# Performance work log

Hardware: AMD Instinct MI355X
Metric: run time of the kernel (lower is better)

The kernel has to match this reference:

```python
import jax, jax.numpy as jnp
import numpy as np
from jax import lax

B, T, C, H, W = 2, 5, 2, 128, 256
E, M, L = 64, 16, 4  # embedding_dim, n_fno_modes, n_fno_layers
EPS = 1e-5


def conv1x1(x, w, b):
    # x: [N, I, H, W], w: [O, I], b: [O]
    return jnp.einsum('nihw,oi->nohw', x, w) + b[None, :, None, None]


def conv3x3(x, w, b):
    # x: [N, I, H, W], w: [O, I, 3, 3]
    y = lax.conv_general_dilated(x, w, window_strides=(1, 1), padding='SAME',
                                 dimension_numbers=('NCHW', 'OIHW', 'NCHW'))
    return y + b[None, :, None, None]


def instance_norm(x):
    # InstanceNorm2d(affine=False): normalize over H,W per (n, c), biased var
    mu = jnp.mean(x, axis=(2, 3), keepdims=True)
    var = jnp.var(x, axis=(2, 3), keepdims=True)
    return (x - mu) * lax.rsqrt(var + EPS)


def upsample2x_nearest(x):
    return jnp.repeat(jnp.repeat(x, 2, axis=2), 2, axis=3)


def resize_nearest(x, out_h, out_w):
    # torch F.interpolate mode='nearest': idx = floor(i * in / out)
    in_h, in_w = x.shape[2], x.shape[3]
    hi = (jnp.arange(out_h) * in_h) // out_h
    wi = (jnp.arange(out_w) * in_w) // out_w
    return x[:, :, hi, :][:, :, :, wi]


def fno_layer(x, wr, wi, cw, cb):
    # x: [N, E, H, W]; wr/wi: [2, E, E, M, M]; cw: [E, E]; cb: [E]
    h, w = x.shape[2], x.shape[3]
    coeff = jnp.fft.rfft2(x, axes=(2, 3), norm='ortho')  # [N, E, H, W//2+1]
    w0 = wr[0] + 1j * wi[0]
    w1 = wr[1] + 1j * wi[1]
    out = jnp.zeros_like(coeff)
    out = out.at[:, :, :M, :M].set(
        jnp.einsum('nixy,ioxy->noxy', coeff[:, :, :M, :M], w0))
    out = out.at[:, :, -M:, :M].set(
        jnp.einsum('nixy,ioxy->noxy', coeff[:, :, -M:, :M], w1))
    spec = jnp.fft.irfft2(out, s=(h, w), axes=(2, 3), norm='ortho')
    return jax.nn.gelu(conv1x1(x, cw, cb) + spec, approximate=False)


def setup_inputs() -> dict:
    key = jax.random.key(0)
    ks = jax.random.split(key, 10)
    s = 0.02
    return {
        'sensor_value': jax.random.normal(ks[0], (B, T, C, H, W), jnp.float32),
        'updim_w': 0.3 * jax.random.normal(ks[1], (E, C), jnp.float32),
        'updim_b': jnp.zeros((E,), jnp.float32),
        'smooth_w': 0.04 * jax.random.normal(ks[2], (E, E, 3, 3), jnp.float32),
        'smooth_b': jnp.zeros((E,), jnp.float32),
        'fno_wr': s * jax.random.normal(ks[3], (L, 2, E, E, M, M), jnp.float32),
        'fno_wi': s * jax.random.normal(ks[4], (L, 2, E, E, M, M), jnp.float32),
        'fno_cw': 0.1 * jax.random.normal(ks[5], (L, E, E), jnp.float32),
        'fno_cb': jnp.zeros((L, E), jnp.float32),
        'downdim_w': 0.1 * jax.random.normal(ks[6], (C, E), jnp.float32),
        'downdim_b': jnp.zeros((C,), jnp.float32),
    }


def reference(sensor_value, updim_w, updim_b, smooth_w, smooth_b,
              fno_wr, fno_wi, fno_cw, fno_cb, downdim_w, downdim_b):
    b, t, c, h, w = sensor_value.shape
    x = sensor_value.reshape(b * t, c, h, w)
    x = conv1x1(x, updim_w, updim_b)
    x = upsample2x_nearest(x)
    x = jax.nn.gelu(instance_norm(conv3x3(x, smooth_w, smooth_b)), approximate=False)
    x = resize_nearest(x, H, W)
    for l in range(L):
        x = fno_layer(x, fno_wr[l], fno_wi[l], fno_cw[l], fno_cb[l])
    x = conv1x1(x, downdim_w, downdim_b)
    return x.reshape(b, t, c, H, W)
```

## Files before the change

### kernel.cpp

```cpp
#include <hip/hip_runtime.h>
#include <math.h>

#define PI_D 3.14159265358979323846


typedef _Float16 h8 __attribute__((ext_vector_type(8)));
typedef float f16v __attribute__((ext_vector_type(16)));

__device__ __forceinline__ float gelu_f(float v){
  return 0.5f*v*(1.0f + erff(v*0.70710678118654752440f));
}

__device__ __forceinline__ int fsw_c(int w){ return (w ^ (w >> 3)) & 7; }

__global__ __launch_bounds__(256) void k_tables_fold(float* __restrict__ twFwH, float* __restrict__ twBwH,
                                                     _Float16* __restrict__ Tspec, _Float16* __restrict__ TdftW,
                                                     const float* __restrict__ smw, const float* __restrict__ upw,
                                                     const float* __restrict__ upb, float* __restrict__ Keff){
  int bid = blockIdx.x;
  if (bid < 96){
    int id = bid*256 + threadIdx.x;
    if (id < 4096){
      int h = id >> 5, m = id & 31;
      int xm = (m < 16) ? m : (96 + m);
      double ang = -2.0*PI_D*(double)((xm*h) & 127)/128.0;
      twFwH[id*2]   = (float)cos(ang);
      twFwH[id*2+1] = (float)sin(ang);
    } else if (id < 8192){
      int j = id - 4096;
      int h = j >> 5, m = j & 31;
      int xm = (m < 16) ? m : (96 + m);
      double ang = 2.0*PI_D*(double)((xm*h) & 127)/128.0;
      twBwH[j*2]   = (float)cos(ang);
      twBwH[j*2+1] = (float)sin(ang);
    } else if (id < 16384){
      int j = id - 8192;
      int w = j >> 5, kk = j & 31;
      int y = kk >> 1;
      double ang = 2.0*PI_D*(double)((w*y) & 255)/256.0;
      double v = (kk & 1) ? -sin(ang) : cos(ang);
      Tspec[j] = (_Float16)v;
    } else if (id < 24576){
      int j = id - 16384;
      int y2 = j >> 8, w = j & 255;
      int y = y2 >> 1;
      double ang = -2.0*PI_D*(double)((w*y) & 255)/256.0;
      double v = (y2 & 1) ? sin(ang) : cos(ang);
      TdftW[j] = (_Float16)v;
    }
  } else {
    int id = (bid-96)*256 + threadIdx.x;
    if (id >= 1024) return;
    int o = id >> 4, rs = (id >> 2) & 3, tap = id & 3;
    int r = rs >> 1, s = rs & 1, a = tap >> 1, b = tap & 1;
    int klo = (r==0) ? (a==0?0:1) : (a==0?0:2);
    int khi = (r==0) ? (a==0?0:2) : (a==0?1:2);
    int llo = (s==0) ? (b==0?0:1) : (b==0?0:2);
    int lhi = (s==0) ? (b==0?0:2) : (b==0?1:2);
    float a0=0.f, a1=0.f, ab=0.f;
    for (int i=0;i<64;++i){
      float t = 0.f;
      for (int kh=klo; kh<=khi; ++kh)
        for (int kw=llo; kw<=lhi; ++kw)
          t += smw[((size_t)o*64+i)*9 + kh*3+kw];
      a0 += t*upw[i*2];
      a1 += t*upw[i*2+1];
      ab += t*upb[i];
    }
    *(float4*)(Keff + o*64 + (rs*4+tap)*4) = make_float4(a0, a1, ab, 0.f);
  }
}

__global__ __launch_bounds__(256) void k_transW(const float* __restrict__ wr, const float* __restrict__ wi,
                                                unsigned* __restrict__ Wt){
  __shared__ unsigned P[64*257];
  int lb = blockIdx.x;
  int i = lb & 63, blk = (lb>>6)&1, l = lb>>7;
  int tid = threadIdx.x;
  size_t sbase = (size_t)l*2097152 + (size_t)blk*1048576 + (size_t)i*16384 + tid;
  for (int o=0;o<64;++o){
    float a = wr[sbase + (size_t)o*256];
    float b = wi[sbase + (size_t)o*256];
    union { unsigned u; _Float16 h[2]; } pk;
    pk.h[0] = (_Float16)a; pk.h[1] = (_Float16)b;
    P[o*257 + tid] = pk.u;
  }
  __syncthreads();
  int o = tid & 63, g = tid >> 6;
  size_t dbase = (size_t)(l*2+blk)*1048576;
  for (int it=0; it<64; ++it){
    int my = g*64 + it;
    Wt[dbase + (size_t)my*4096 + i*64 + o] = P[o*257 + my];
  }
}

__global__ __launch_bounds__(512) void k_corrbnd(const float* __restrict__ sv, float* __restrict__ Rpart,
                                                 float* __restrict__ Bnd){
  __shared__ float SH[3120];
  int bid = blockIdx.x;
  int tid = threadIdx.x;
  if (bid < 320){
    int band = bid & 31, n = bid >> 5;
    int u0 = band*4;
    for (int t = tid; t < 3120; t += 512){
      int ch = t / 1560; int rem = t - ch*1560; int rr = rem / 260; int ci = rem - rr*260;
      int row = u0 - 1 + rr, col = ci - 1;
      float v = 0.f;
      if (row >= 0 && row < 128 && col >= 0 && col < 256)
        v = sv[((size_t)(n*2+ch)*128 + row)*256 + col];
      SH[(ch*6+rr)*260 + ci] = v;
    }
    __syncthreads();

    int lane = tid & 63, wv = tid >> 6;
    int c  = (wv<4) ? (wv>>1) : ((wv<6) ? (wv-4) : 2);
    int c2 = (wv<4) ? (wv&1)  : ((wv<6) ? 2 : (wv-6));
    float acc[9];
    #pragma unroll
    for (int k=0;k<9;++k) acc[k]=0.f;

    for (int r=0;r<4;++r){
      int u = u0 + r, lu = r + 1;
      for (int cb=0;cb<4;++cb){
        int v = cb*64 + lane;
        float f = (c==2) ? 1.f : SH[(c*6+lu)*260 + 1+v];
        #pragma unroll
        for (int dr=-1;dr<=1;++dr){
          int ur = u + dr;
          float rko = (ur>=0 && ur<128) ? 1.f : 0.f;
          #pragma unroll
          for (int dc=-1;dc<=1;++dc){
            float g;
            if (c2==2){
              int vc = v + dc;
              g = rko * ((vc>=0 && vc<256) ? 1.f : 0.f);
            } else {
              g = SH[(c2*6+lu+dr)*260 + 1+v+dc];
            }
            acc[(dr+1)*3 + dc+1] += f*g;
          }
        }
      }
    }
    #pragma unroll
    for (int k=0;k<9;++k){
      float v = acc[k];
      for (int off=32; off; off>>=1) v += __shfl_xor(v, off);
      if (lane==0) Rpart[((size_t)(n*32+band)*8 + wv)*9 + k] = v;
    }
  } else {
    int n = bid - 320;
    for (int t = tid; t < 3120; t += 512){
      int e = t/780; int rem = t - e*780; int ch = rem/260; int i = rem - ch*260;
      int idx = i - 1;
      int len = (e<2) ? 256 : 128;
      float v = 0.f;
      if (idx >= 0 && idx < len){
        if (ch==2) v = 1.f;
        else {
          int row = (e==0) ? 0 : (e==1) ? 127 : idx;
          int col = (e==2) ? 0 : (e==3) ? 255 : idx;
          v = sv[((size_t)(n*2+ch)*128 + row)*256 + col];
        }
      }
      SH[(e*3+ch)*260 + i] = v;
    }
    __syncthreads();
    if (tid < 108){
      int e = tid/27; int rem = tid - e*27; int pair = rem/3; int lag = rem%3 - 1;
      int c = pair/3, c2 = pair%3;
      int len = (e<2) ? 256 : 128;
      float a = 0.f;
      for (int i=0;i<len;++i) a += SH[(e*3+c)*260 + 1+i]*SH[(e*3+c2)*260 + 1+i+lag];
      Bnd[n*144 + tid] = a;
    } else if (tid < 144){
      int t = tid - 108; int corner = t/9; int pair = t - corner*9;
      int c = pair/3, c2 = pair%3;
      int e = (corner<2) ? 0 : 1;
      int idx = (corner&1) ? 255 : 0;
      Bnd[n*144 + tid] = SH[(e*3+c)*260 + 1+idx]*SH[(e*3+c2)*260 + 1+idx];
    }
  }
}

__global__ __launch_bounds__(256) void k_stats3(const float* __restrict__ Rpart, const float* __restrict__ Bnd,
                                                const float* __restrict__ Keff, float* __restrict__ stats){
  __shared__ float R[9][9];
  __shared__ float BL[4][9][3];
  __shared__ float CR[4][9];
  __shared__ float M[4][12][12];
  int n = blockIdx.x, tid = threadIdx.x;

  if (tid < 72){
    int wv = tid/9, k = tid - (tid/9)*9;
    double s = 0.0;
    for (int b=0;b<32;++b) s += (double)Rpart[((size_t)(n*32+b)*8 + wv)*9 + k];
    int c  = (wv<4) ? (wv>>1) : ((wv<6) ? (wv-4) : 2);
    int c2 = (wv<4) ? (wv&1)  : ((wv<6) ? 2 : (wv-6));
    R[c*3+c2][k] = (float)s;
  } else if (tid < 81){
    int k = tid - 72; int dr = k/3 - 1, dc = k%3 - 1;
    R[8][k] = (float)((128 - (dr<0?-dr:dr)) * (256 - (dc<0?-dc:dc)));
  }
  if (tid < 108){
    int e = tid/27, rem = tid - (tid/27)*27;
    BL[e][rem/3][rem%3] = Bnd[n*144 + tid];
  } else if (tid < 144){
    int t = tid - 108;
    CR[t/9][t - (t/9)*9] = Bnd[n*144 + tid];
  }
  __syncthreads();

  for (int t = tid; t < 576; t += 256){
    int rs = t/144; int rem = t - rs*144; int i = rem/12, j = rem - (rem/12)*12;
    int ab = i/3,  c  = i - ab*3,  a  = ab>>1, b  = ab&1;
    int ab2 = j/3, c2 = j - ab2*3, a2 = ab2>>1, b2 = ab2&1;
    int r = rs>>1, s = rs&1;
    int dr = a2 - a, dc = b2 - b;
    int pair = c*3 + c2;
    float g = R[pair][(dr+1)*3 + (dc+1)];
    if (r==1 && a==1 && a2==1) g -= BL[0][pair][dc+1];
    if (r==0 && a==0 && a2==0) g -= BL[1][pair][dc+1];
    if (s==1 && b==1 && b2==1) g -= BL[2][pair][dr+1];
    if (s==0 && b==0 && b2==0) g -= BL[3][pair][dr+1];
    bool rowc = (a==a2) && ((r==1 && a==1) || (r==0 && a==0));
    bool colc = (b==b2) && ((s==1 && b==1) || (s==0 && b==0));
    if (rowc && colc){
      int corner = ((r==1)?0:2) + ((s==1)?0:1);
      g += CR[corner][pair];
    }
    M[rs][i][j] = g;
  }
  __syncthreads();

  if (tid < 64){
    int o = tid;
    double S1 = 0.0, S2 = 0.0;
    for (int rs=0; rs<4; ++rs){
      float w[12];
      #pragma unroll
      for (int ab=0; ab<4; ++ab){
        float4 kv = *(const float4*)(Keff + o*64 + (rs*4+ab)*4);
        w[ab*3+0] = kv.x; w[ab*3+1] = kv.y; w[ab*3+2] = kv.z;
      }
      #pragma unroll
      for (int i=0;i<12;++i){
        double ti = 0.0;
        #pragma unroll
        for (int j=0;j<12;++j) ti += (double)M[rs][i][j]*(double)w[j];
        S2 += (double)w[i]*ti;
      }
      #pragma unroll
      for (int ab=0; ab<4; ++ab)
        #pragma unroll
        for (int c=0;c<3;++c)
          S1 += (double)w[ab*3+c]*(double)M[rs][ab*3+c][ab*3+2];
    }
    double mu  = S1 / 131072.0;
    double var = S2 / 131072.0 - mu*mu;
    stats[(n*64+o)*2]   = (float)mu;
    stats[(n*64+o)*2+1] = (float)(1.0/sqrt(var + 1e-5));
  }
}

__global__ __launch_bounds__(256) void k_convnorm(const float* __restrict__ sv,
                                                  const float* __restrict__ Keff,
                                                  const float* __restrict__ stats,
                                                  _Float16* __restrict__ act){
  __shared__ float SV[4*260];
  int bid = blockIdx.x;
  int p = bid & 127, n = bid >> 7;
  int tid = threadIdx.x;
  for (int t = tid; t < 1032; t += 256){
    int dr = t / 516;
    int rem = t - dr*516;
    int ch = rem / 258;
    int ci = rem - ch*258;
    int row = p - 1 + dr;
    int col = ci - 1;
    float v = 0.f;
    if (row >= 0 && col >= 0 && col < 256)
      v = sv[((size_t)(n*2+ch)*128 + row)*256 + col];
    SV[(dr*2+ch)*260 + ci] = v;
  }
  __syncthreads();

  int q = tid;
  float x0[4], x1[4], ib[4];
  float rowok0 = (p>0)?1.f:0.f;
  float colok0 = (q>0)?1.f:0.f;
  #pragma unroll
  for (int a=0;a<2;++a)
    #pragma unroll
    for (int b=0;b<2;++b){
      x0[a*2+b] = SV[(a*2+0)*260 + q + b];
      x1[a*2+b] = SV[(a*2+1)*260 + q + b];
      ib[a*2+b] = (a==0?rowok0:1.f) * (b==0?colok0:1.f);
    }

  for (int o=0; o<64; ++o){
    const float4* kp = (const float4*)(Keff + o*64);
    float y = 0.f;
    #pragma unroll
    for (int t=0;t<4;++t){
      float4 kv = kp[t];
      y += kv.x*x0[t] + kv.y*x1[t] + kv.z*ib[t];
    }
    float mu = stats[(n*64+o)*2], istd = stats[(n*64+o)*2+1];
    float v = (y - mu)*istd;
    act[((size_t)(n*64+o)*128 + p)*256 + q] = (_Float16)gelu_f(v);
  }
}

__global__ __launch_bounds__(256, 2) void k_dftW_mfma(const _Float16* __restrict__ act,
                                                      const _Float16* __restrict__ TdftW,
                                                      float* __restrict__ Cy){
  __shared__ _Float16 Ax[32768];
  __shared__ _Float16 Bt[8192];
  int tid = threadIdx.x;
  int hp = blockIdx.x & 63, n = blockIdx.x >> 6;
  int h0 = hp*2;

  {
    int a = tid >> 1;
    int ws = (tid & 1) * 128;
    int e = a & 63, ht = a >> 6;
    const _Float16* src = act + ((size_t)(n*64+e))*32768 + (size_t)(h0+ht)*256 + ws;
    #pragma unroll
    for (int k=0;k<16;++k){
      h8 v = *(const h8*)(src + k*8);
      int wq = (ws >> 3) + k;
      int chunk = wq ^ (a & 7);
      *(h8*)(Ax + a*256 + chunk*8) = v;
    }
  }
  {
    int y2 = tid & 31, ws = (tid >> 5) * 32;
    const _Float16* src = TdftW + y2*256 + ws;
    #pragma unroll
    for (int k=0;k<4;++k){
      h8 v = *(const h8*)(src + k*8);
      int wq = (ws >> 3) + k;
      int chunk = wq ^ (y2 & 7);
      *(h8*)(Bt + y2*256 + chunk*8) = v;
    }
  }
  __syncthreads();

  int lane = tid & 63;
  int l31 = lane & 31, l5 = lane >> 5;
  int mt = tid >> 6;
  int a = mt*32 + l31;

  f16v acc;
  #pragma unroll
  for (int j=0;j<16;++j) acc[j] = 0.f;
  #pragma unroll
  for (int ks=0;ks<16;++ks){
    int kb = ks*16 + l5*8;
    int cA = (kb>>3) ^ (a & 7);
    int cB = (kb>>3) ^ (l31 & 7);
    h8 af = *(const h8*)(Ax + a*256 + cA*8);
    h8 bf = *(const h8*)(Bt + l31*256 + cB*8);
    acc = __builtin_amdgcn_mfma_f32_32x32x16_f16(bf, af, acc, 0,0,0);
  }
  int e = a & 63, ht = a >> 6;
  #pragma unroll
  for (int j=0;j<16;j+=2){
    int y2 = (j&3) + 8*(j>>2) + 4*l5;
    int yy = y2 >> 1;
    *(float2*)(Cy + (((size_t)(n*16+yy)*128 + h0+ht)*64 + e)*2) = make_float2(acc[j], acc[j+1]);
  }
}

__global__ __launch_bounds__(256) void k_specAB(const float* __restrict__ Cy,
                                                const float* __restrict__ twF,
                                                const unsigned* __restrict__ Wt,
                                                float* __restrict__ MS, int l){
  __shared__ float CO[8*64*2];
  int bid = blockIdx.x;
  int mq = bid / 160;
  int pid = bid - mq*160;
  int y = pid & 15, n = pid >> 4;
  int tid = threadIdx.x;
  int lane = tid & 63;
  int wv = __builtin_amdgcn_readfirstlane(tid >> 6);

  {
    int m0 = mq*8 + wv*2;
    const float* cyb = Cy + (((size_t)(n*16+y)*128)*64 + lane)*2;
    const float* tf = twF + m0*2;
    float ar0=0.f, ai0=0.f, ar1=0.f, ai1=0.f;
    for (int h=0; h<128; ++h){
      float2 c = *(const float2*)(cyb + h*128);
      const float* tp = tf + h*64;
      float t0r = tp[0], t0i = tp[1], t1r = tp[2], t1i = tp[3];
      ar0 += t0r*c.x - t0i*c.y; ai0 += t0r*c.y + t0i*c.x;
      ar1 += t1r*c.x - t1i*c.y; ai1 += t1r*c.y + t1i*c.x;
    }
    int mm = wv*2;
    *(float2*)(CO + (mm*64 + lane)*2)     = make_float2(ar0, ai0);
    *(float2*)(CO + ((mm+1)*64 + lane)*2) = make_float2(ar1, ai1);
  }
  __syncthreads();

  {
    #pragma unroll
    for (int t2=0; t2<2; ++t2){
      int mm = wv*2 + t2;
      int m = mq*8 + mm;
      int blk = m >> 4, mloc = m & 15;
      int my = mloc*16 + y;
      const unsigned* wb = Wt + ((size_t)((l*2+blk)*256 + my))*4096 + lane;
      float mr = 0.f, mi = 0.f;
      for (int i=0;i<64;++i){
        float2 cc = *(const float2*)(CO + (mm*64 + i)*2);
        union { unsigned u; _Float16 h[2]; } pk;
        pk.u = wb[(size_t)i*64];
        float wr_f = (float)pk.h[0], wi_f = (float)pk.h[1];
        mr += cc.x*wr_f - cc.y*wi_f;
        mi += cc.x*wi_f + cc.y*wr_f;
      }
      *(float2*)(MS + (((size_t)(n*16+y)*32 + m)*64 + lane)*2) = make_float2(mr, mi);
    }
  }
}

__global__ __launch_bounds__(256) void k_specC(const float* __restrict__ MS,
                                               const float* __restrict__ twB,
                                               float* __restrict__ G){
  __shared__ float SM[32*64*2];
  int bid = blockIdx.x;
  int hq = bid / 160;
  int pid = bid - hq*160;
  int y = pid & 15, n = pid >> 4;
  int tid = threadIdx.x;
  int lane = tid & 63;
  int wv = __builtin_amdgcn_readfirstlane(tid >> 6);

  {
    const float4* src = (const float4*)(MS + ((size_t)(n*16+y)*32)*128);
    float4* dst = (float4*)SM;
    #pragma unroll
    for (int t=0; t<4; ++t) dst[tid + t*256] = src[tid + t*256];
  }
  __syncthreads();

  float f = (y==0) ? (1.f/32768.f) : (2.f/32768.f);
  for (int k=0;k<8;++k){
    int h = hq*32 + wv*8 + k;
    const float* tb = twB + h*64;
    float gr=0.f, gi=0.f;
    #pragma unroll
    for (int m=0;m<32;++m){
      float tr = tb[m*2], ti = tb[m*2+1];
      float2 mo2 = *(const float2*)(SM + (m*64+lane)*2);
      gr += tr*mo2.x - ti*mo2.y;
      gi += tr*mo2.y + ti*mo2.x;
    }
    size_t gb = (((size_t)(n*128+h)*16 + y)*2)*64 + lane;
    G[gb]      = gr*f;
    G[gb + 64] = gi*f;
  }
}

__global__ __launch_bounds__(1024, 8) void k_combine_mfma(const _Float16* __restrict__ act_in,
                                                          const float* __restrict__ G,
                                                          const _Float16* __restrict__ Tspec,
                                                          const _Float16* __restrict__ TdftW,
                                                          const float* __restrict__ cw,
                                                          const float* __restrict__ cb,
                                                          const float* __restrict__ wd,
                                                          const float* __restrict__ bd,
                                                          _Float16* __restrict__ act_out,
                                                          float* __restrict__ Cy,
                                                          float* __restrict__ outp,
                                                          int flags){
  __shared__ __align__(16) _Float16 Lh[40960];
  _Float16* Bx = Lh;
  _Float16* At = Lh + 32768;
  int tid = threadIdx.x;
  int h = blockIdx.x & 127, n = blockIdx.x >> 7;

  {
    int rp = tid >> 5, sub = tid & 31;
    int i0 = 2*rp;
    int wbase = sub*8;
    const _Float16* r0 = act_in + (size_t)(n*64+i0)*32768 + (size_t)h*256 + wbase;
    const _Float16* r1 = r0 + 32768;
    h8 A0 = *(const h8*)r0;
    h8 B0 = *(const h8*)r1;
    int cbs = rp >> 2;
    int lo  = i0 & 7;
    #pragma unroll
    for (int k=0;k<8;++k){
      union { _Float16 hh[2]; unsigned u; } pk;
      pk.hh[0] = A0[k];
      pk.hh[1] = B0[k];
      int w = wbase + k;
      int chunk = cbs ^ fsw_c(w);
      *(unsigned*)(Bx + w*128 + chunk*8 + lo) = pk.u;
    }
  }
  if (tid < 512){
    int o = tid >> 3, seg = (tid & 7)*8;
    float4 c0 = *(const float4*)(cw + o*64 + seg);
    float4 c1 = *(const float4*)(cw + o*64 + seg + 4);
    h8 v;
    v[0]=(_Float16)c0.x; v[1]=(_Float16)c0.y; v[2]=(_Float16)c0.z; v[3]=(_Float16)c0.w;
    v[4]=(_Float16)c1.x; v[5]=(_Float16)c1.y; v[6]=(_Float16)c1.z; v[7]=(_Float16)c1.w;
    int ch0 = (seg>>3) ^ (o & 7);
    *(h8*)(At + o*128 + ch0*8) = v;
  } else {
    int t5 = tid - 512;
    const float* gp = G + (size_t)(n*128 + h)*2048 + t5*4;
    float4 g = *(const float4*)gp;
    float gvx[4] = {g.x, g.y, g.z, g.w};
    int idx0 = t5*4;
    int yc = idx0 >> 6;
    int o0 = idx0 & 63;
    int kk = 64 + yc;
    #pragma unroll
    for (int j=0;j<4;++j){
      int o = o0 + j;
      int chunk = (kk >> 3) ^ (o & 7);
      At[o*128 + chunk*8 + (kk & 7)] = (_Float16)gvx[j];
    }
  }
  if (tid < 512){
    int w = tid >> 1, half = tid & 1;
    const _Float16* tp = Tspec + w*32 + half*16;
    #pragma unroll
    for (int c=0;c<2;++c){
      h8 v = *(const h8*)(tp + c*8);
      int cc = half*2 + c;
      int chunk = (8 + cc) ^ fsw_c(w);
      *(h8*)(Bx + w*128 + chunk*8) = v;
    }
  }
  __syncthreads();

  int lane = tid & 63;
  int l31 = lane & 31, l5 = lane >> 5;
  int w0i = tid >> 6;
  int mt = w0i & 1, ng = w0i >> 1;
  int o_lane = mt*32 + l31;

  h8 af[6];
  #pragma unroll
  for (int ks=0;ks<6;++ks){
    int kb = ks*16 + l5*8;
    int chunk = (kb>>3) ^ (o_lane & 7);
    af[ks] = *(const h8*)(At + o_lane*128 + chunk*8);
  }

  f16v acc;
  #pragma unroll
  for (int j=0;j<16;++j) acc[j] = cb[mt*32 + (j&3) + 8*(j>>2) + 4*l5];

  {
    int w = ng*32 + l31;
    const _Float16* bbase = Bx + w*128;
    int wf = fsw_c(w);
    #pragma unroll
    for (int ks=0;ks<6;++ks){
      int kb = ks*16 + l5*8;
      int chunk = (kb>>3) ^ wf;
      h8 bf = *(const h8*)(bbase + chunk*8);
      acc = __builtin_amdgcn_mfma_f32_32x32x16_f16(af[ks], bf, acc, 0,0,0);
    }
  }

  float gvv[16];
  #pragma unroll
  for (int j=0;j<16;++j) gvv[j] = gelu_f(acc[j]);

  int wcol = ng*32 + l31;
  if (flags != 2){
    #pragma unroll
    for (int j=0;j<16;++j){
      int o = mt*32 + (j&3) + 8*(j>>2) + 4*l5;
      act_out[(size_t)(n*64+o)*32768 + (size_t)h*256 + wcol] = (_Float16)gvv[j];
    }
  }
  __syncthreads();

  if (flags == 1){
    _Float16* gL  = Lh;
    _Float16* TdL = Lh + 16384;
    {
      int wc3 = wcol >> 3, wc7 = wcol & 7;
      #pragma unroll
      for (int j=0;j<16;++j){
        int o = mt*32 + (j&3) + 8*(j>>2) + 4*l5;
        gL[o*256 + ((wc3 ^ (o & 7))*8) + wc7] = (_Float16)gvv[j];
      }
    }
    {
      int y2 = tid & 31, ws = (tid >> 5)*8;
      const _Float16* src = TdftW + y2*256 + ws;
      h8 v = *(const h8*)src;
      int chunk = (ws>>3) ^ (y2 & 7);
      *(h8*)(TdL + y2*256 + chunk*8) = v;
    }
    __syncthreads();
    float* P = (float*)(Lh + 24576);
    if (w0i < 8){
      int mt2 = w0i & 1, kq = w0i >> 1;
      int ocol = mt2*32 + l31;
      f16v acc2;
      #pragma unroll
      for (int j=0;j<16;++j) acc2[j] = 0.f;
      #pragma unroll
      for (int ks=0;ks<4;++ks){
        int kb = (kq*4+ks)*16 + l5*8;
        h8 af2 = *(const h8*)(gL  + ocol*256 + (((kb>>3) ^ (ocol & 7))*8));
        h8 bf2 = *(const h8*)(TdL + l31*256  + (((kb>>3) ^ (l31 & 7))*8));
        acc2 = __builtin_amdgcn_mfma_f32_32x32x16_f16(bf2, af2, acc2, 0,0,0);
      }
      #pragma unroll
      for (int j=0;j<16;++j){
        int y2 = (j&3) + 8*(j>>2) + 4*l5;
        P[w0i*1024 + y2*32 + l31] = acc2[j];
      }
    }
    __syncthreads();
    {
      int yy = tid >> 6, o = tid & 63, mt2 = o >> 5, o31 = o & 31;
      float re = P[(0*2+mt2)*1024 + (2*yy)*32 + o31]   + P[(1*2+mt2)*1024 + (2*yy)*32 + o31]
               + P[(2*2+mt2)*1024 + (2*yy)*32 + o31]   + P[(3*2+mt2)*1024 + (2*yy)*32 + o31];
      float im = P[(0*2+mt2)*1024 + (2*yy+1)*32 + o31] + P[(1*2+mt2)*1024 + (2*yy+1)*32 + o31]
               + P[(2*2+mt2)*1024 + (2*yy+1)*32 + o31] + P[(3*2+mt2)*1024 + (2*yy+1)*32 + o31];
      *(float2*)(Cy + (((size_t)(n*16+yy)*128 + h)*64 + o)*2) = make_float2(re, im);
    }
  } else {
    float p0=0.f, p1=0.f;
    #pragma unroll
    for (int j=0;j<16;++j){
      int o = mt*32 + (j&3) + 8*(j>>2) + 4*l5;
      p0 += wd[o]*gvv[j];
      p1 += wd[64+o]*gvv[j];
    }
    p0 += __shfl_xor(p0,32);
    p1 += __shfl_xor(p1,32);
    float* red = (float*)(Lh + 32768);
    if (l5 == 0){
      red[wcol*4 + mt*2 + 0] = p0;
      red[wcol*4 + mt*2 + 1] = p1;
    }
    __syncthreads();
    if (tid < 512){
      int ch = tid >> 8, wc = tid & 255;
      float v = red[wc*4 + ch] + red[wc*4 + 2 + ch] + bd[ch];
      outp[(size_t)n*65536 + (size_t)ch*32768 + (size_t)h*256 + wc] = v;
    }
  }
}

extern "C" void kernel_launch(void* const* d_in, const int* in_sizes, int n_in,
                              void* d_out, int out_size, void* d_ws, size_t ws_size,
                              hipStream_t stream) {
  const float* sv  = (const float*)d_in[0];
  const float* upw = (const float*)d_in[1];
  const float* upb = (const float*)d_in[2];
  const float* smw = (const float*)d_in[3];
  const float* smb = (const float*)d_in[4];
  const float* fwr = (const float*)d_in[5];
  const float* fwi = (const float*)d_in[6];
  const float* fcw = (const float*)d_in[7];
  const float* fcb = (const float*)d_in[8];
  const float* ddw = (const float*)d_in[9];
  const float* ddb = (const float*)d_in[10];
  float* out = (float*)d_out;
  (void)smb;

  float* W = (float*)d_ws;
  _Float16* actA = (_Float16*)W;
  _Float16* actB = (_Float16*)(W + 10485760);
  float* Cy    = W + 20971520;
  float* G     = W + 23592960;
  float* part  = W + 26214400;
  float* stats = W + 28180480;
  float* Keff  = W + 28181760;
  float* twFwH = W + 28185856;
  float* twBwH = W + 28194048;
  _Float16* Tspec = (_Float16*)(W + 28202240);
  _Float16* TdftW = (_Float16*)(W + 28206336);
  unsigned* Wt   = (unsigned*)(W + 28210432);

  float* Rpart = part;
  float* Bnd   = part + 30000;
  float* MS    = part + 65536;

  k_tables_fold<<<100,256,0,stream>>>(twFwH, twBwH, Tspec, TdftW, smw, upw, upb, Keff);
  k_transW<<<512,256,0,stream>>>(fwr, fwi, Wt);
  k_corrbnd<<<330,512,0,stream>>>(sv, Rpart, Bnd);
  k_stats3<<<10,256,0,stream>>>(Rpart, Bnd, Keff, stats);
  k_convnorm<<<1280,256,0,stream>>>(sv, Keff, stats, actA);
  k_dftW_mfma<<<640,256,0,stream>>>(actA, TdftW, Cy);

  _Float16* xa = actA; _Float16* xb = actB;
  for (int l=0;l<4;++l){
    k_specAB<<<640,256,0,stream>>>(Cy, twFwH, Wt, MS, l);
    k_specC<<<640,256,0,stream>>>(MS, twBwH, G);
    k_combine_mfma<<<1280,1024,0,stream>>>(xa, G, Tspec, TdftW,
                                           fcw + (size_t)l*4096, fcb + (size_t)l*64,
                                           ddw, ddb, xb, Cy, out, (l<3)?1:2);
    _Float16* t = xa; xa = xb; xb = t;
  }
}
```

Measured before the change: 466.7 us.

## Fuse W-direction DFT into convnorm and inverse H-DFT into combine, switch to NHWC

```diff
diff --git a/kernel.cpp b/kernel.cpp
--- a/kernel.cpp
+++ b/kernel.cpp
@@ -5,6 +5,7 @@
 
 
 typedef _Float16 h8 __attribute__((ext_vector_type(8)));
+typedef _Float16 h4v __attribute__((ext_vector_type(4)));
 typedef float f16v __attribute__((ext_vector_type(16)));
 
 __device__ __forceinline__ float gelu_f(float v){
@@ -263,15 +264,21 @@
   }
 }
 
-__global__ __launch_bounds__(256) void k_convnorm(const float* __restrict__ sv,
-                                                  const float* __restrict__ Keff,
-                                                  const float* __restrict__ stats,
-                                                  _Float16* __restrict__ act){
-  __shared__ float SV[4*260];
+__global__ __launch_bounds__(1024, 8) void k_convnorm(const float* __restrict__ sv,
+                                                      const float* __restrict__ Keff,
+                                                      const float* __restrict__ stats,
+                                                      const _Float16* __restrict__ TdftW,
+                                                      _Float16* __restrict__ act,
+                                                      float* __restrict__ Cy){
+  __shared__ __align__(16) _Float16 Lh[40960];
+  _Float16* gL  = Lh;
+  _Float16* TdL = Lh + 16384;
+  float*    P   = (float*)(Lh + 24576);
+  float*    SV  = P;
   int bid = blockIdx.x;
   int p = bid & 127, n = bid >> 7;
   int tid = threadIdx.x;
-  for (int t = tid; t < 1032; t += 256){
+  for (int t = tid; t < 1032; t += 1024){
     int dr = t / 516;
     int rem = t - dr*516;
     int ch = rem / 258;
@@ -283,9 +290,17 @@
       v = sv[((size_t)(n*2+ch)*128 + row)*256 + col];
     SV[(dr*2+ch)*260 + ci] = v;
   }
-  __syncthreads();
-
-  int q = tid;
+  {
+    int y2 = tid & 31, ws = (tid >> 5)*8;
+    const _Float16* src = TdftW + y2*256 + ws;
+    h8 v = *(const h8*)src;
+    int chunk = (ws>>3) ^ (y2 & 7);
+    *(h8*)(TdL + y2*256 + chunk*8) = v;
+  }
+  __syncthreads();
+
+  int q = tid & 255;
+  int og = __builtin_amdgcn_readfirstlane(tid >> 8);
   float x0[4], x1[4], ib[4];
   float rowok0 = (p>0)?1.f:0.f;
   float colok0 = (q>0)?1.f:0.f;
@@ -298,7 +313,11 @@
       ib[a*2+b] = (a==0?rowok0:1.f) * (b==0?colok0:1.f);
     }
 
-  for (int o=0; o<64; ++o){
+  union { _Float16 g16[16]; h8 gv8[2]; } U;
+  int q3 = q>>3, q7 = q&7;
+  #pragma unroll
+  for (int oi=0; oi<16; ++oi){
+    int o = og*16 + oi;
     const float4* kp = (const float4*)(Keff + o*64);
     float y = 0.f;
     #pragma unroll
@@ -307,69 +326,47 @@
       y += kv.x*x0[t] + kv.y*x1[t] + kv.z*ib[t];
     }
     float mu = stats[(n*64+o)*2], istd = stats[(n*64+o)*2+1];
-    float v = (y - mu)*istd;
-    act[((size_t)(n*64+o)*128 + p)*256 + q] = (_Float16)gelu_f(v);
-  }
-}
-
-__global__ __launch_bounds__(256, 2) void k_dftW_mfma(const _Float16* __restrict__ act,
-                                                      const _Float16* __restrict__ TdftW,
-                                                      float* __restrict__ Cy){
-  __shared__ _Float16 Ax[32768];
-  __shared__ _Float16 Bt[8192];
-  int tid = threadIdx.x;
-  int hp = blockIdx.x & 63, n = blockIdx.x >> 6;
-  int h0 = hp*2;
-
-  {
-    int a = tid >> 1;
-    int ws = (tid & 1) * 128;
-    int e = a & 63, ht = a >> 6;
-    const _Float16* src = act + ((size_t)(n*64+e))*32768 + (size_t)(h0+ht)*256 + ws;
-    #pragma unroll
-    for (int k=0;k<16;++k){
-      h8 v = *(const h8*)(src + k*8);
-      int wq = (ws >> 3) + k;
-      int chunk = wq ^ (a & 7);
-      *(h8*)(Ax + a*256 + chunk*8) = v;
-    }
-  }
-  {
-    int y2 = tid & 31, ws = (tid >> 5) * 32;
-    const _Float16* src = TdftW + y2*256 + ws;
-    #pragma unroll
-    for (int k=0;k<4;++k){
-      h8 v = *(const h8*)(src + k*8);
-      int wq = (ws >> 3) + k;
-      int chunk = wq ^ (y2 & 7);
-      *(h8*)(Bt + y2*256 + chunk*8) = v;
-    }
+    _Float16 gh = (_Float16)gelu_f((y - mu)*istd);
+    U.g16[oi] = gh;
+    gL[o*256 + ((q3 ^ (o & 7))*8) + q7] = gh;
+  }
+  {
+    _Float16* ap = act + (((size_t)(n*128+p)*256 + q)*64 + og*16);
+    *(h8*)ap = U.gv8[0];
+    *(h8*)(ap+8) = U.gv8[1];
   }
   __syncthreads();
 
   int lane = tid & 63;
   int l31 = lane & 31, l5 = lane >> 5;
-  int mt = tid >> 6;
-  int a = mt*32 + l31;
-
-  f16v acc;
-  #pragma unroll
-  for (int j=0;j<16;++j) acc[j] = 0.f;
-  #pragma unroll
-  for (int ks=0;ks<16;++ks){
-    int kb = ks*16 + l5*8;
-    int cA = (kb>>3) ^ (a & 7);
-    int cB = (kb>>3) ^ (l31 & 7);
-    h8 af = *(const h8*)(Ax + a*256 + cA*8);
-    h8 bf = *(const h8*)(Bt + l31*256 + cB*8);
-    acc = __builtin_amdgcn_mfma_f32_32x32x16_f16(bf, af, acc, 0,0,0);
-  }
-  int e = a & 63, ht = a >> 6;
-  #pragma unroll
-  for (int j=0;j<16;j+=2){
-    int y2 = (j&3) + 8*(j>>2) + 4*l5;
-    int yy = y2 >> 1;
-    *(float2*)(Cy + (((size_t)(n*16+yy)*128 + h0+ht)*64 + e)*2) = make_float2(acc[j], acc[j+1]);
+  int w0i = tid >> 6;
+  if (w0i < 8){
+    int mt2 = w0i & 1, kq = w0i >> 1;
+    int ocol = mt2*32 + l31;
+    f16v acc2;
+    #pragma unroll
+    for (int j=0;j<16;++j) acc2[j] = 0.f;
+    #pragma unroll
+    for (int ks=0;ks<4;++ks){
+      int kb = (kq*4+ks)*16 + l5*8;
+      h8 af2 = *(const h8*)(gL  + ocol*256 + (((kb>>3) ^ (ocol & 7))*8));
+      h8 bf2 = *(const h8*)(TdL + l31*256  + (((kb>>3) ^ (l31 & 7))*8));
+      acc2 = __builtin_amdgcn_mfma_f32_32x32x16_f16(bf2, af2, acc2, 0,0,0);
+    }
+    #pragma unroll
+    for (int j=0;j<16;++j){
+      int y2 = (j&3) + 8*(j>>2) + 4*l5;
+      P[w0i*1024 + y2*32 + l31] = acc2[j];
+    }
+  }
+  __syncthreads();
+  {
+    int yy = tid >> 6, o = tid & 63, mt2 = o >> 5, o31 = o & 31;
+    float re = P[(0*2+mt2)*1024 + (2*yy)*32 + o31]   + P[(1*2+mt2)*1024 + (2*yy)*32 + o31]
+             + P[(2*2+mt2)*1024 + (2*yy)*32 + o31]   + P[(3*2+mt2)*1024 + (2*yy)*32 + o31];
+    float im = P[(0*2+mt2)*1024 + (2*yy+1)*32 + o31] + P[(1*2+mt2)*1024 + (2*yy+1)*32 + o31]
+             + P[(2*2+mt2)*1024 + (2*yy+1)*32 + o31] + P[(3*2+mt2)*1024 + (2*yy+1)*32 + o31];
+    *(float2*)(Cy + (((size_t)(n*16+yy)*128 + p)*64 + o)*2) = make_float2(re, im);
   }
 }
 
@@ -405,6 +402,7 @@
   __syncthreads();
 
   {
+    float f = (y==0) ? (1.f/32768.f) : (2.f/32768.f);
     #pragma unroll
     for (int t2=0; t2<2; ++t2){
       int mm = wv*2 + t2;
@@ -421,53 +419,16 @@
         mr += cc.x*wr_f - cc.y*wi_f;
         mi += cc.x*wi_f + cc.y*wr_f;
       }
-      *(float2*)(MS + (((size_t)(n*16+y)*32 + m)*64 + lane)*2) = make_float2(mr, mi);
-    }
-  }
-}
-
-__global__ __launch_bounds__(256) void k_specC(const float* __restrict__ MS,
-                                               const float* __restrict__ twB,
-                                               float* __restrict__ G){
-  __shared__ float SM[32*64*2];
-  int bid = blockIdx.x;
-  int hq = bid / 160;
-  int pid = bid - hq*160;
-  int y = pid & 15, n = pid >> 4;
-  int tid = threadIdx.x;
-  int lane = tid & 63;
-  int wv = __builtin_amdgcn_readfirstlane(tid >> 6);
-
-  {
-    const float4* src = (const float4*)(MS + ((size_t)(n*16+y)*32)*128);
-    float4* dst = (float4*)SM;
-    #pragma unroll
-    for (int t=0; t<4; ++t) dst[tid + t*256] = src[tid + t*256];
-  }
-  __syncthreads();
-
-  float f = (y==0) ? (1.f/32768.f) : (2.f/32768.f);
-  for (int k=0;k<8;++k){
-    int h = hq*32 + wv*8 + k;
-    const float* tb = twB + h*64;
-    float gr=0.f, gi=0.f;
-    #pragma unroll
-    for (int m=0;m<32;++m){
-      float tr = tb[m*2], ti = tb[m*2+1];
-      float2 mo2 = *(const float2*)(SM + (m*64+lane)*2);
-      gr += tr*mo2.x - ti*mo2.y;
-      gi += tr*mo2.y + ti*mo2.x;
-    }
-    size_t gb = (((size_t)(n*128+h)*16 + y)*2)*64 + lane;
-    G[gb]      = gr*f;
-    G[gb + 64] = gi*f;
+      *(float2*)(MS + (((size_t)(n*16+y)*32 + m)*64 + lane)*2) = make_float2(mr*f, mi*f);
+    }
   }
 }
 
 __global__ __launch_bounds__(1024, 8) void k_combine_mfma(const _Float16* __restrict__ act_in,
-                                                          const float* __restrict__ G,
+                                                          const float* __restrict__ MS,
                                                           const _Float16* __restrict__ Tspec,
                                                           const _Float16* __restrict__ TdftW,
+                                                          const float* __restrict__ twB,
                                                           const float* __restrict__ cw,
                                                           const float* __restrict__ cb,
                                                           const float* __restrict__ wd,
@@ -482,25 +443,30 @@
   int tid = threadIdx.x;
   int h = blockIdx.x & 127, n = blockIdx.x >> 7;
 
-  {
-    int rp = tid >> 5, sub = tid & 31;
-    int i0 = 2*rp;
-    int wbase = sub*8;
-    const _Float16* r0 = act_in + (size_t)(n*64+i0)*32768 + (size_t)h*256 + wbase;
-    const _Float16* r1 = r0 + 32768;
-    h8 A0 = *(const h8*)r0;
-    h8 B0 = *(const h8*)r1;
-    int cbs = rp >> 2;
-    int lo  = i0 & 7;
-    #pragma unroll
-    for (int k=0;k<8;++k){
-      union { _Float16 hh[2]; unsigned u; } pk;
-      pk.hh[0] = A0[k];
-      pk.hh[1] = B0[k];
-      int w = wbase + k;
-      int chunk = cbs ^ fsw_c(w);
-      *(unsigned*)(Bx + w*128 + chunk*8 + lo) = pk.u;
-    }
+  int wA = tid >> 2, ksg = tid & 3;
+  const _Float16* asrc = act_in + (((size_t)(n*128+h)*256 + wA)*64 + ksg*16);
+  h8 av0 = *(const h8*)asrc;
+  h8 av1 = *(const h8*)(asrc + 8);
+
+  int o_g = tid & 63;
+  int yv = __builtin_amdgcn_readfirstlane(tid >> 6);
+  float gr = 0.f, gi = 0.f;
+  {
+    const float* ms = MS + (size_t)(n*16+yv)*4096 + o_g*2;
+    const float* tb = twB + h*64;
+    #pragma unroll 4
+    for (int m=0;m<32;++m){
+      float tr = tb[m*2], ti = tb[m*2+1];
+      float2 mo = *(const float2*)(ms + m*128);
+      gr += tr*mo.x - ti*mo.y;
+      gi += tr*mo.y + ti*mo.x;
+    }
+  }
+
+  {
+    int fw = fsw_c(wA);
+    *(h8*)(Bx + wA*128 + ((ksg*2)   ^ fw)*8) = av0;
+    *(h8*)(Bx + wA*128 + ((ksg*2+1) ^ fw)*8) = av1;
   }
   if (tid < 512){
     int o = tid >> 3, seg = (tid & 7)*8;
@@ -513,30 +479,21 @@
     *(h8*)(At + o*128 + ch0*8) = v;
   } else {
     int t5 = tid - 512;
-    const float* gp = G + (size_t)(n*128 + h)*2048 + t5*4;
-    float4 g = *(const float4*)gp;
-    float gvx[4] = {g.x, g.y, g.z, g.w};
-    int idx0 = t5*4;
-    int yc = idx0 >> 6;
-    int o0 = idx0 & 63;
-    int kk = 64 + yc;
-    #pragma unroll
-    for (int j=0;j<4;++j){
-      int o = o0 + j;
-      int chunk = (kk >> 3) ^ (o & 7);
-      At[o*128 + chunk*8 + (kk & 7)] = (_Float16)gvx[j];
-    }
-  }
-  if (tid < 512){
-    int w = tid >> 1, half = tid & 1;
+    int w = t5 >> 1, half = t5 & 1;
     const _Float16* tp = Tspec + w*32 + half*16;
+    int fw = fsw_c(w);
     #pragma unroll
     for (int c=0;c<2;++c){
       h8 v = *(const h8*)(tp + c*8);
       int cc = half*2 + c;
-      int chunk = (8 + cc) ^ fsw_c(w);
-      *(h8*)(Bx + w*128 + chunk*8) = v;
-    }
+      *(h8*)(Bx + w*128 + ((8 + cc) ^ fw)*8) = v;
+    }
+  }
+  {
+    int kk0 = 64 + 2*yv;
+    At[o_g*128 + (((kk0>>3) ^ (o_g & 7))*8) + (kk0 & 7)] = (_Float16)gr;
+    int kk1 = kk0 + 1;
+    At[o_g*128 + (((kk1>>3) ^ (o_g & 7))*8) + (kk1 & 7)] = (_Float16)gi;
   }
   __syncthreads();
 
@@ -558,10 +515,10 @@
   #pragma unroll
   for (int j=0;j<16;++j) acc[j] = cb[mt*32 + (j&3) + 8*(j>>2) + 4*l5];
 
-  {
-    int w = ng*32 + l31;
-    const _Float16* bbase = Bx + w*128;
-    int wf = fsw_c(w);
+  int wcol = ng*32 + l31;
+  {
+    const _Float16* bbase = Bx + wcol*128;
+    int wf = fsw_c(wcol);
     #pragma unroll
     for (int ks=0;ks<6;++ks){
       int kb = ks*16 + l5*8;
@@ -575,12 +532,14 @@
   #pragma unroll
   for (int j=0;j<16;++j) gvv[j] = gelu_f(acc[j]);
 
-  int wcol = ng*32 + l31;
   if (flags != 2){
-    #pragma unroll
-    for (int j=0;j<16;++j){
-      int o = mt*32 + (j&3) + 8*(j>>2) + 4*l5;
-      act_out[(size_t)(n*64+o)*32768 + (size_t)h*256 + wcol] = (_Float16)gvv[j];
+    _Float16* ab = act_out + (((size_t)(n*128+h)*256 + wcol)*64 + mt*32 + 4*l5);
+    #pragma unroll
+    for (int g=0;g<4;++g){
+      h4v v4;
+      v4[0]=(_Float16)gvv[g*4+0]; v4[1]=(_Float16)gvv[g*4+1];
+      v4[2]=(_Float16)gvv[g*4+2]; v4[3]=(_Float16)gvv[g*4+3];
+      *(h4v*)(ab + 8*g) = v4;
     }
   }
   __syncthreads();
@@ -678,7 +637,6 @@
   _Float16* actA = (_Float16*)W;
   _Float16* actB = (_Float16*)(W + 10485760);
   float* Cy    = W + 20971520;
-  float* G     = W + 23592960;
   float* part  = W + 26214400;
   float* stats = W + 28180480;
   float* Keff  = W + 28181760;
@@ -696,14 +654,12 @@
   k_transW<<<512,256,0,stream>>>(fwr, fwi, Wt);
   k_corrbnd<<<330,512,0,stream>>>(sv, Rpart, Bnd);
   k_stats3<<<10,256,0,stream>>>(Rpart, Bnd, Keff, stats);
-  k_convnorm<<<1280,256,0,stream>>>(sv, Keff, stats, actA);
-  k_dftW_mfma<<<640,256,0,stream>>>(actA, TdftW, Cy);
+  k_convnorm<<<1280,1024,0,stream>>>(sv, Keff, stats, TdftW, actA, Cy);
 
   _Float16* xa = actA; _Float16* xb = actB;
   for (int l=0;l<4;++l){
     k_specAB<<<640,256,0,stream>>>(Cy, twFwH, Wt, MS, l);
-    k_specC<<<640,256,0,stream>>>(MS, twBwH, G);
-    k_combine_mfma<<<1280,1024,0,stream>>>(xa, G, Tspec, TdftW,
+    k_combine_mfma<<<1280,1024,0,stream>>>(xa, MS, Tspec, TdftW, twBwH,
                                            fcw + (size_t)l*4096, fcb + (size_t)l*64,
                                            ddw, ddb, xb, Cy, out, (l<3)?1:2);
     _Float16* t = xa; xa = xb; xb = t;
```

Measured after the change: 482.4 us. 1.03x slower.
